# Performance work log

Measured on AMD Instinct MI355X. Metric: run time of the kernel, lower is better.

Reference implementation:

```python
import jax, jax.numpy as jnp
import numpy as np

B, N, F = 8, 2048, 64
H, LAT = 256, 64
K1, K2 = N // 2, N // 4  # DiffPool keeps nodes//2 per stage


def _adj_mm(A, x):
    # A: [N,M] (shared) or [B,N,M] (per-sample); x: [B,M,F]
    if A.ndim == 2:
        return jnp.einsum('nm,bmf->bnf', A, x)
    return jnp.einsum('bnm,bmf->bnf', A, x)


def _gcn(x, A, W, b, act=None):
    # spektral GCNConv: act(A @ (X W) + b)
    h = _adj_mm(A, x @ W) + b
    return act(h) if act is not None else h


def _diffpool(x, A, K_emb, K_pool):
    # spektral DiffPool (linear embedding activation, softmax selection)
    z = _adj_mm(A, x @ K_emb)                               # [B,N,C]
    s = jax.nn.softmax(_adj_mm(A, x @ K_pool), axis=-1)     # [B,N,K]
    x_pool = jnp.einsum('bnk,bnc->bkc', s, z)               # S^T Z
    AS = _adj_mm(A, s)                                       # [B,N,K]
    A_pool = jnp.einsum('bnk,bnl->bkl', s, AS)              # S^T A S
    return x_pool, A_pool, s


def setup_inputs() -> dict:
    key = jax.random.key(0)
    ks = jax.random.split(key, 24)

    def glorot(k, shape):
        return (jax.random.normal(k, shape) * jnp.sqrt(2.0 / (shape[0] + shape[1]))).astype(jnp.float32)

    # symmetric sparse-ish adjacency with self loops, GCN-normalized (keeps activations stable)
    mask = (jax.random.uniform(ks[0], (N, N)) < 0.01).astype(jnp.float32)
    A = jnp.minimum(jnp.maximum(mask, mask.T) + jnp.eye(N, dtype=jnp.float32), 1.0)
    dinv = 1.0 / jnp.sqrt(jnp.sum(A, axis=-1))
    adj = A * dinv[:, None] * dinv[None, :]

    return {
        'x': jax.random.normal(ks[1], (B, N, F), dtype=jnp.float32),
        'eps': jax.random.normal(ks[2], (B, K2, LAT), dtype=jnp.float32),
        'adj': adj,
        'We1': glorot(ks[3], (F, H)), 'be1': jnp.zeros((H,), jnp.float32),
        'Kemb1': glorot(ks[4], (H, H)), 'Kpool1': glorot(ks[5], (H, K1)),
        'We2': glorot(ks[6], (H, H)), 'be2': jnp.zeros((H,), jnp.float32),
        'Kemb2': glorot(ks[7], (H, H)), 'Kpool2': glorot(ks[8], (H, K2)),
        'We3': glorot(ks[9], (H, 2 * LAT)), 'be3': jnp.zeros((2 * LAT,), jnp.float32),
        'Wd0': glorot(ks[10], (LAT, H)), 'bd0': jnp.zeros((H,), jnp.float32),
        'Wd1': glorot(ks[11], (H, H)), 'bd1': jnp.zeros((H,), jnp.float32),
        'Wd2': glorot(ks[12], (H, H)), 'bd2': jnp.zeros((H,), jnp.float32),
        'Wdf': glorot(ks[13], (H, F)), 'bdf': jnp.zeros((F,), jnp.float32),
    }


def reference(x, eps, adj, We1, be1, Kemb1, Kpool1, We2, be2, Kemb2, Kpool2,
              We3, be3, Wd0, bd0, Wd1, bd1, Wd2, bd2, Wdf, bdf):
    A0 = adj
    # ---- encode ----
    h = _gcn(x, A0, We1, be1, jax.nn.relu)              # [B,N,H]
    h, A1, s1 = _diffpool(h, A0, Kemb1, Kpool1)          # [B,K1,H], [B,K1,K1], [B,N,K1]
    h = _gcn(h, A1, We2, be2, jax.nn.relu)
    h, A2, s2 = _diffpool(h, A1, Kemb2, Kpool2)          # [B,K2,H]
    h = _gcn(h, A2, We3, be3, None)                      # [B,K2,2*LAT]
    mean, log_var = jnp.split(h, 2, axis=-1)
    z = mean + jnp.exp(0.5 * log_var) * eps              # reparameterize
    # ---- decode ----
    d = _gcn(z, A2, Wd0, bd0, jax.nn.relu)
    d = jnp.einsum('bnk,bkc->bnc', s2, d)                # DiffUnpool: S @ x
    d = _gcn(d, A1, Wd1, bd1, jax.nn.relu)
    d = jnp.einsum('bnk,bkc->bnc', s1, d)
    d = _gcn(d, A0, Wd2, bd2, jax.nn.relu)
    out = _gcn(d, A0, Wdf, bdf, jax.nn.softplus)         # [B,N,F]
    return out, mean, log_var
```

## Files before the change

### kernel.cpp

```cpp
#include <hip/hip_runtime.h>
#include <math.h>

#define BATCH 8
typedef unsigned short US;

typedef __attribute__((ext_vector_type(8))) short short8;
typedef __attribute__((ext_vector_type(4))) float f32x4;

__device__ __forceinline__ US f2b(float f) {
  union { float f; unsigned u; } v; v.f = f;
  unsigned r = v.u + 0x7fffu + ((v.u >> 16) & 1u);
  return (US)(r >> 16);
}
__device__ __forceinline__ float b2f(US h) {
  union { unsigned u; float f; } v; v.u = ((unsigned)h) << 16;
  return v.f;
}

__device__ __forceinline__ void gload16(const US* g, US* l) {
  __builtin_amdgcn_global_load_lds(
      (const __attribute__((address_space(1))) unsigned int*)g,
      (__attribute__((address_space(3))) unsigned int*)l, 16, 0, 0);
}

__device__ __forceinline__ int lidx2(int r, int ko) {
  return r * 64 + ((((ko >> 3) ^ (r & 7)) << 3));
}

template <int TN, int ACT, int OUT, bool HASBIAS>
__global__ __launch_bounds__(256) void mm_k(
    const US* __restrict__ A, const US* __restrict__ B,
    const float* __restrict__ bias, void* __restrict__ Cv, void* __restrict__ Cv2,
    int M, int N, int K, int lda, long long sA, long long sB, long long sC,
    long long sC2, int gx, int gy) {
  constexpr int JF = TN / 32;
  __shared__ US As[128 * 64];
  __shared__ US Bs[TN * 64];

  const int nb = blockIdx.x;
  const int nb2 = (nb & 7) * (gx * gy) + (nb >> 3);
  const int bx = nb2 % gx;
  const int by = (nb2 / gx) % gy;
  const int b = nb2 / (gx * gy);

  A += (long long)b * sA;
  B += (long long)b * sB;
  const int m0 = by * 128, n0 = bx * TN;
  const int t = threadIdx.x, lane = t & 63, w = t >> 6;
  const int wm = (w >> 1) * 64, wn = (w & 1) * (TN / 2);
  const int l15 = lane & 15, lg = lane >> 4;
  const int lrow = lane >> 3;
  const int gcell = (((lane & 7) ^ lrow) << 3);

  f32x4 acc[4][JF];
#pragma unroll
  for (int i = 0; i < 4; ++i)
#pragma unroll
    for (int j = 0; j < JF; ++j) acc[i][j] = (f32x4){0.f, 0.f, 0.f, 0.f};

  for (int k0 = 0; k0 < K; k0 += 64) {
#pragma unroll
    for (int i = 0; i < 4; ++i) {
      const int g = w * 4 + i;
      gload16(A + (long long)(m0 + g * 8 + lrow) * lda + k0 + gcell, &As[g * 512]);
    }
#pragma unroll
    for (int i = 0; i < TN / 32; ++i) {
      const int g = w * (TN / 32) + i;
      gload16(B + (long long)(n0 + g * 8 + lrow) * K + k0 + gcell, &Bs[g * 512]);
    }
    __syncthreads();

#pragma unroll
    for (int kk = 0; kk < 2; ++kk) {
      const int ko = kk * 32 + lg * 8;
      short8 af[4], bf[JF];
#pragma unroll
      for (int i = 0; i < 4; ++i)
        af[i] = *(const short8*)&As[lidx2(wm + i * 16 + l15, ko)];
#pragma unroll
      for (int j = 0; j < JF; ++j)
        bf[j] = *(const short8*)&Bs[lidx2(wn + j * 16 + l15, ko)];
#pragma unroll
      for (int i = 0; i < 4; ++i)
#pragma unroll
        for (int j = 0; j < JF; ++j)
          acc[i][j] = __builtin_amdgcn_mfma_f32_16x16x32_bf16(af[i], bf[j],
                                                              acc[i][j], 0, 0, 0);
    }
    __syncthreads();
  }

  const long long cb = (long long)b * sC;
  const long long cb2 = (long long)b * sC2;
#pragma unroll
  for (int fj = 0; fj < JF; ++fj) {
    const int col = n0 + wn + fj * 16 + l15;
    const float bsv = HASBIAS ? bias[col] : 0.0f;
#pragma unroll
    for (int fi = 0; fi < 4; ++fi) {
      const int row0 = m0 + wm + fi * 16 + lg * 4;
      float v[4];
#pragma unroll
      for (int e = 0; e < 4; ++e) {
        float x = acc[fi][fj][e] + bsv;
        if (ACT == 1) x = fmaxf(x, 0.0f);
        if (ACT == 2) x = (x > 20.0f) ? x : log1pf(expf(x));
        v[e] = x;
      }
      if (OUT == 1 || OUT == 3) {
        ushort4 pk;
        pk.x = f2b(v[0]); pk.y = f2b(v[1]); pk.z = f2b(v[2]); pk.w = f2b(v[3]);
        US* c2 = (OUT == 3) ? (US*)Cv2 : (US*)Cv;
        *(ushort4*)&c2[cb2 + (long long)col * M + row0] = pk;
      }
      if (OUT == 0 || OUT == 3) {
#pragma unroll
        for (int e = 0; e < 4; ++e)
          ((US*)Cv)[cb + (long long)(row0 + e) * N + col] = f2b(v[e]);
      }
      if (OUT == 2) {
#pragma unroll
        for (int e = 0; e < 4; ++e)
          ((float*)Cv)[cb + (long long)(row0 + e) * N + col] = v[e];
      }
    }
  }
}

template <int OUT>
__global__ __launch_bounds__(512, 1) void mm256_k(
    const US* __restrict__ A, const US* __restrict__ B, void* __restrict__ Cv,
    void* __restrict__ Cv2, int M, int N, int K, int lda, long long sA,
    long long sB, long long sC, long long sC2, int gx, int gy) {
  __shared__ US lds[8][8192];

  const int nb = blockIdx.x;
  const int chunk = gx * gy;
  const int nb2 = (nb & 7) * chunk + (nb >> 3);
  const int bx = nb2 % gx;
  const int by = (nb2 / gx) % gy;
  const int b = nb2 / chunk;

  const int m0 = by * 256, n0 = bx * 256;
  const int tid = threadIdx.x;
  const int lane = tid & 63, w = tid >> 6;
  const int wr = w >> 2, wc = w & 3;
  const int l15 = lane & 15, lg = lane >> 4;

  const US* Ab = A + (long long)b * sA + (long long)m0 * lda;
  const US* Bb = B + (long long)b * sB + (long long)n0 * K;
  const int NT = K >> 6;

  auto stageH = [&](int H) {
    const int s = H >> 2, h = H & 3;
    const int ab = h & 1, kk = h >> 1;
    US* reg = &lds[ab * 4 + (s & 1) * 2 + kk][0];
    const US* src = ab ? Bb : Ab;
    const int ld = ab ? K : lda;
#pragma unroll
    for (int i = 0; i < 2; ++i) {
      const int rbase = (w * 2 + i) * 16;
      const int r = rbase + (lane >> 2);
      const int csrc = (lane & 3) ^ ((r >> 1) & 3);
      gload16(src + (long long)r * ld + s * 64 + kk * 32 + csrc * 8,
              reg + rbase * 32);
    }
  };

  f32x4 acc[8][4];
#pragma unroll
  for (int m = 0; m < 8; ++m)
#pragma unroll
    for (int j = 0; j < 4; ++j) acc[m][j] = (f32x4){0.f, 0.f, 0.f, 0.f};
  short8 a4[4], b4[4];

  for (int H = 0; H < 6; ++H) stageH(H);
  asm volatile("s_waitcnt vmcnt(4)" ::: "memory");
  __builtin_amdgcn_s_barrier();

#define PH(kk_, mh_, DOH, HV, VM, tt)                                          \
  {                                                                            \
    const US* Ar = &lds[((tt) & 1) * 2 + (kk_)][0];                            \
    const US* Br = &lds[4 + ((tt) & 1) * 2 + (kk_)][0];                        \
    _Pragma("unroll") for (int i = 0; i < 4; ++i) {                            \
      const int r = wr * 128 + (mh_) * 64 + i * 16 + l15;                      \
      a4[i] = *(const short8*)&Ar[r * 32 + ((lg ^ ((r >> 1) & 3)) << 3)];      \
    }                                                                          \
    if ((mh_) == 0) {                                                          \
      _Pragma("unroll") for (int j = 0; j < 4; ++j) {                          \
        const int rr = wc * 64 + j * 16 + l15;                                 \
        b4[j] = *(const short8*)&Br[rr * 32 + ((lg ^ ((rr >> 1) & 3)) << 3)];  \
      }                                                                        \
    }                                                                          \
    if (DOH) stageH(HV);                                                       \
    if ((VM) == 1) asm volatile("s_waitcnt vmcnt(4)" ::: "memory");            \
    if ((VM) == 2) asm volatile("s_waitcnt vmcnt(0)" ::: "memory");            \
    __builtin_amdgcn_s_barrier();                                              \
    __builtin_amdgcn_s_setprio(1);                                             \
    _Pragma("unroll") for (int i = 0; i < 4; ++i)                              \
      _Pragma("unroll") for (int j = 0; j < 4; ++j)                            \
        acc[(mh_) * 4 + i][j] = __builtin_amdgcn_mfma_f32_16x16x32_bf16(       \
            a4[i], b4[j], acc[(mh_) * 4 + i][j], 0, 0, 0);                     \
    __builtin_amdgcn_s_setprio(0);                                             \
    __builtin_amdgcn_s_barrier();                                              \
  }

  int t2 = 0;
  for (; t2 < NT - 2; ++t2) {
    PH(0, 0, true, 4 * t2 + 6, 0, t2)
    PH(0, 1, true, 4 * t2 + 7, 0, t2)
    PH(1, 0, true, 4 * t2 + 8, 0, t2)
    PH(1, 1, true, 4 * t2 + 9, 1, t2)
  }
  PH(0, 0, true, 4 * (NT - 2) + 6, 0, NT - 2)
  PH(0, 1, true, 4 * (NT - 2) + 7, 0, NT - 2)
  PH(1, 0, false, 0, 0, NT - 2)
  PH(1, 1, false, 0, 2, NT - 2)
  PH(0, 0, false, 0, 0, NT - 1)
  PH(0, 1, false, 0, 0, NT - 1)
  PH(1, 0, false, 0, 0, NT - 1)
  PH(1, 1, false, 0, 0, NT - 1)
#undef PH

  const long long cb = (long long)b * sC;
  const long long cb2 = (long long)b * sC2;
#pragma unroll
  for (int j = 0; j < 4; ++j) {
    const int col = n0 + wc * 64 + j * 16 + l15;
#pragma unroll
    for (int m = 0; m < 8; ++m) {
      const int row0 = m0 + wr * 128 + m * 16 + lg * 4;
      if (OUT == 1 || OUT == 3) {
        ushort4 pk;
        pk.x = f2b(acc[m][j][0]); pk.y = f2b(acc[m][j][1]);
        pk.z = f2b(acc[m][j][2]); pk.w = f2b(acc[m][j][3]);
        US* c2 = (OUT == 3) ? (US*)Cv2 : (US*)Cv;
        *(ushort4*)&c2[cb2 + (long long)col * M + row0] = pk;
      }
      if (OUT == 0 || OUT == 3) {
#pragma unroll
        for (int e = 0; e < 4; ++e)
          ((US*)Cv)[cb + (long long)(row0 + e) * N + col] = f2b(acc[m][j][e]);
      }
    }
  }
}

template <int ACT, int OUT, bool HASBIAS>
__global__ __launch_bounds__(256) void mm64_k(
    const US* __restrict__ A, const US* __restrict__ B,
    const float* __restrict__ bias, void* __restrict__ Cv,
    int M, int N, int K, int lda, long long sA, long long sB, long long sC,
    int gx, int gy) {
  __shared__ US As[4][4096];
  __shared__ US Bs[4][4096];

  const int nb = blockIdx.x;
  const int chunk = gx * gy;
  const int nb2 = (nb & 7) * chunk + (nb >> 3);
  const int bx = nb2 % gx;
  const int by = (nb2 / gx) % gy;
  const int b = nb2 / chunk;

  const int m0 = by * 64, n0 = bx * 64;
  const int tid = threadIdx.x;
  const int lane = tid & 63, w = tid >> 6;
  const int wr = w >> 1, wc = w & 1;
  const int l15 = lane & 15, lg = lane >> 4;
  const int lrow = lane >> 3;
  const int gcell = (((lane & 7) ^ lrow) << 3);

  const US* Ag = A + (long long)b * sA + (long long)m0 * lda;
  const US* Bg = B + (long long)b * sB + (long long)n0 * K;
  const int NT = K >> 6;

  auto stage = [&](int tt) {
    US* Ad = &As[tt & 3][0];
    US* Bd = &Bs[tt & 3][0];
    const int k0 = tt * 64;
#pragma unroll
    for (int i = 0; i < 2; ++i) {
      const int g = w * 2 + i;
      const int r = g * 8 + lrow;
      gload16(Ag + (long long)r * lda + k0 + gcell, Ad + g * 512);
      gload16(Bg + (long long)r * K + k0 + gcell, Bd + g * 512);
    }
  };

  f32x4 acc[2][2];
#pragma unroll
  for (int i = 0; i < 2; ++i)
#pragma unroll
    for (int j = 0; j < 2; ++j) acc[i][j] = (f32x4){0.f, 0.f, 0.f, 0.f};

  for (int i = 0; i < 3 && i < NT; ++i) stage(i);

  for (int t = 0; t < NT; ++t) {
    if (t + 3 < NT) stage(t + 3);
    const int rem = NT - 1 - t;
    if (rem >= 3) asm volatile("s_waitcnt vmcnt(12)" ::: "memory");
    else if (rem == 2) asm volatile("s_waitcnt vmcnt(8)" ::: "memory");
    else if (rem == 1) asm volatile("s_waitcnt vmcnt(4)" ::: "memory");
    else asm volatile("s_waitcnt vmcnt(0)" ::: "memory");
    asm volatile("s_barrier" ::: "memory");
    const US* Ad = &As[t & 3][0];
    const US* Bd = &Bs[t & 3][0];
#pragma unroll
    for (int kk = 0; kk < 2; ++kk) {
      const int ko = kk * 32 + lg * 8;
      short8 af[2], bf[2];
      af[0] = *(const short8*)&Ad[lidx2(wr * 32 + l15, ko)];
      af[1] = *(const short8*)&Ad[lidx2(wr * 32 + 16 + l15, ko)];
      bf[0] = *(const short8*)&Bd[lidx2(wc * 32 + l15, ko)];
      bf[1] = *(const short8*)&Bd[lidx2(wc * 32 + 16 + l15, ko)];
#pragma unroll
      for (int i = 0; i < 2; ++i)
#pragma unroll
        for (int j = 0; j < 2; ++j)
          acc[i][j] = __builtin_amdgcn_mfma_f32_16x16x32_bf16(af[i], bf[j],
                                                              acc[i][j], 0, 0, 0);
    }
    asm volatile("s_barrier" ::: "memory");
  }

  const long long cb = (long long)b * sC;
#pragma unroll
  for (int fj = 0; fj < 2; ++fj) {
    const int col = n0 + wc * 32 + fj * 16 + l15;
    const float bsv = HASBIAS ? bias[col] : 0.0f;
#pragma unroll
    for (int fi = 0; fi < 2; ++fi) {
      const int row0 = m0 + wr * 32 + fi * 16 + lg * 4;
      float v[4];
#pragma unroll
      for (int e = 0; e < 4; ++e) {
        float x = acc[fi][fj][e] + bsv;
        if (ACT == 1) x = fmaxf(x, 0.0f);
        if (ACT == 2) x = (x > 20.0f) ? x : log1pf(expf(x));
        v[e] = x;
      }
      if (OUT == 1) {
        ushort4 pk;
        pk.x = f2b(v[0]); pk.y = f2b(v[1]); pk.z = f2b(v[2]); pk.w = f2b(v[3]);
        *(ushort4*)&((US*)Cv)[cb + (long long)col * M + row0] = pk;
      } else if (OUT == 0) {
#pragma unroll
        for (int e = 0; e < 4; ++e)
          ((US*)Cv)[cb + (long long)(row0 + e) * N + col] = f2b(v[e]);
      } else {
#pragma unroll
        for (int e = 0; e < 4; ++e)
          ((float*)Cv)[cb + (long long)(row0 + e) * N + col] = v[e];
      }
    }
  }
}

__global__ __launch_bounds__(256) void csr_count_k(const float* __restrict__ adj,
                                                   int* __restrict__ rowcnt) {
  const int row = blockIdx.x, t = threadIdx.x;
  const float* p = adj + (long long)row * 2048;
  int c = 0;
  for (int j = t; j < 2048; j += 256) c += (p[j] != 0.0f);
  __shared__ int red[256];
  red[t] = c;
  __syncthreads();
  for (int s = 128; s; s >>= 1) {
    if (t < s) red[t] += red[t + s];
    __syncthreads();
  }
  if (t == 0) rowcnt[row] = red[0];
}

__global__ __launch_bounds__(256) void csr_scan_k(const int* __restrict__ rowcnt,
                                                  int* __restrict__ rowptr) {
  __shared__ int red[256];
  const int t = threadIdx.x;
  int base = 0;
  for (int ch = 0; ch < 8; ++ch) {
    const int v = rowcnt[ch * 256 + t];
    red[t] = v;
    __syncthreads();
    for (int s = 1; s < 256; s <<= 1) {
      const int add = (t >= s) ? red[t - s] : 0;
      __syncthreads();
      red[t] += add;
      __syncthreads();
    }
    rowptr[ch * 256 + t] = base + red[t] - v;
    const int tot = red[255];
    __syncthreads();
    base += tot;
  }
  if (t == 0) rowptr[2048] = base;
}

__global__ __launch_bounds__(256) void csr_fill_k(const float* __restrict__ adj,
                                                  const int* __restrict__ rowptr,
                                                  int* __restrict__ colidx,
                                                  float* __restrict__ vals) {
  const int row = blockIdx.x, t = threadIdx.x;
  const float* p = adj + (long long)row * 2048;
  int cnt = 0;
  for (int j = t; j < 2048; j += 256) cnt += (p[j] != 0.0f);
  __shared__ int red[256];
  red[t] = cnt;
  __syncthreads();
  for (int s = 1; s < 256; s <<= 1) {
    const int add = (t >= s) ? red[t - s] : 0;
    __syncthreads();
    red[t] += add;
    __syncthreads();
  }
  int off = rowptr[row] + red[t] - cnt;
  for (int j = t; j < 2048; j += 256) {
    const float a = p[j];
    if (a != 0.0f) {
      colidx[off] = j;
      vals[off] = a;
      ++off;
    }
  }
}

template <int COLS, bool INF32, int ACT, bool OUTF32, bool HASBIAS>
__global__ __launch_bounds__(256) void spmm_k(
    const int* __restrict__ rowptr, const int* __restrict__ colidx,
    const float* __restrict__ vals, const void* __restrict__ Xv,
    const float* __restrict__ bias, void* __restrict__ Yv) {
  constexpr int BP = 256 / COLS;
  constexpr int NP = BATCH / BP;
  const int row = blockIdx.x;
  const int t = threadIdx.x;
  const int c = t & (COLS - 1);
  const int bsub = t / COLS;
  const int e0 = rowptr[row], e1 = rowptr[row + 1];
  float acc[NP];
#pragma unroll
  for (int p = 0; p < NP; ++p) acc[p] = 0.0f;
  for (int e = e0; e < e1; ++e) {
    const int j = colidx[e];
    const float a = vals[e];
#pragma unroll
    for (int p = 0; p < NP; ++p) {
      const int b = p * BP + bsub;
      const long long idx = ((long long)b * 2048 + j) * COLS + c;
      const float xv = INF32 ? ((const float*)Xv)[idx] : b2f(((const US*)Xv)[idx]);
      acc[p] += a * xv;
    }
  }
#pragma unroll
  for (int p = 0; p < NP; ++p) {
    const int b = p * BP + bsub;
    float v = acc[p] + (HASBIAS ? bias[c] : 0.0f);
    if (ACT == 2) v = (v > 20.0f) ? v : log1pf(expf(v));
    const long long idx = ((long long)b * 2048 + row) * COLS + c;
    if (OUTF32) ((float*)Yv)[idx] = v;
    else ((US*)Yv)[idx] = f2b(v);
  }
}

template <int RPT>
__global__ __launch_bounds__(256) void sm_partial_k(
    const US* __restrict__ x, float* __restrict__ pm, float* __restrict__ ps,
    int R, int C, long long sB, int NS) {
  const int b = blockIdx.y, blk = blockIdx.x;
  const int cpr = C >> 3;
  const int t = threadIdx.x;
  const int cslot = t & (cpr - 1);
  const int rsub = t / cpr;
  const int nsub = 256 / cpr;
  const int rowsPerBlock = R / NS;
  const int r0 = blk * rowsPerBlock + rsub * RPT;
  const US* p = x + (long long)b * sB + (long long)r0 * C + cslot * 8;
  union { uint4 v; US s[8]; } buf[RPT];
#pragma unroll
  for (int i = 0; i < RPT; ++i) buf[i].v = *(const uint4*)(p + (long long)i * C);
  float M[8], S[8];
#pragma unroll
  for (int j = 0; j < 8; ++j) M[j] = b2f(buf[0].s[j]);
#pragma unroll
  for (int i = 1; i < RPT; ++i)
#pragma unroll
    for (int j = 0; j < 8; ++j) M[j] = fmaxf(M[j], b2f(buf[i].s[j]));
#pragma unroll
  for (int j = 0; j < 8; ++j) S[j] = 0.f;
#pragma unroll
  for (int i = 0; i < RPT; ++i)
#pragma unroll
    for (int j = 0; j < 8; ++j) S[j] += __expf(b2f(buf[i].s[j]) - M[j]);
  const long long pi = (long long)(b * NS + blk) * nsub + rsub;
  float* pmo = pm + pi * C + cslot * 8;
  float* pso = ps + pi * C + cslot * 8;
  *(float4*)pmo = make_float4(M[0], M[1], M[2], M[3]);
  *(float4*)(pmo + 4) = make_float4(M[4], M[5], M[6], M[7]);
  *(float4*)pso = make_float4(S[0], S[1], S[2], S[3]);
  *(float4*)(pso + 4) = make_float4(S[4], S[5], S[6], S[7]);
}

__global__ __launch_bounds__(256) void sm_combine_k(
    const float* __restrict__ pm, const float* __restrict__ ps,
    float* __restrict__ Mf, float* __restrict__ Sinv, int C, int NP) {
  const int b = blockIdx.x, t = threadIdx.x;
  const int cpr = C >> 3;
  if (t >= cpr) return;
  const int c = t * 8;
  const float* pmB = pm + (long long)b * NP * C + c;
  const float* psB = ps + (long long)b * NP * C + c;
  float M[8], S[8];
#pragma unroll
  for (int j = 0; j < 8; ++j) { M[j] = pmB[j]; S[j] = psB[j]; }
  for (int e = 1; e < NP; ++e) {
    const float* pme = pmB + (long long)e * C;
    const float* pse = psB + (long long)e * C;
#pragma unroll
    for (int j = 0; j < 8; ++j) {
      const float m2 = pme[j], s2 = pse[j];
      const float nm = fmaxf(M[j], m2);
      S[j] = S[j] * __expf(M[j] - nm) + s2 * __expf(m2 - nm);
      M[j] = nm;
    }
  }
#pragma unroll
  for (int j = 0; j < 8; ++j) {
    Mf[(long long)b * C + c + j] = M[j];
    Sinv[(long long)b * C + c + j] = 1.0f / S[j];
  }
}

template <int RPT>
__global__ __launch_bounds__(256) void sm_norm_k(
    US* __restrict__ x, const float* __restrict__ Mf,
    const float* __restrict__ Sinv, int R, int C, long long sB, int NS) {
  const int b = blockIdx.y, blk = blockIdx.x;
  const int cpr = C >> 3;
  const int t = threadIdx.x;
  const int cslot = t & (cpr - 1);
  const int rsub = t / cpr;
  const int rowsPerBlock = R / NS;
  const int r0 = blk * rowsPerBlock + rsub * RPT;
  US* p = x + (long long)b * sB + (long long)r0 * C + cslot * 8;
  float M[8], Si[8];
#pragma unroll
  for (int j = 0; j < 8; ++j) {
    M[j] = Mf[(long long)b * C + cslot * 8 + j];
    Si[j] = Sinv[(long long)b * C + cslot * 8 + j];
  }
#pragma unroll
  for (int i = 0; i < RPT; ++i) {
    union { uint4 v; US s[8]; } buf;
    buf.v = *(const uint4*)(p + (long long)i * C);
#pragma unroll
    for (int j = 0; j < 8; ++j)
      buf.s[j] = f2b(__expf(b2f(buf.s[j]) - M[j]) * Si[j]);
    *(uint4*)(p + (long long)i * C) = buf.v;
  }
}

struct WT { const float* src; US* dst; int R, C, tileOff; };
struct WTab { WT e[11]; };

__global__ __launch_bounds__(256) void wtrans_k(WTab tab) {
  __shared__ US L[64][65];
  const int tile = blockIdx.x;
  int i = 0;
#pragma unroll
  for (int j = 1; j < 11; ++j)
    if (tab.e[j].tileOff <= tile) i = j;
  const WT w = tab.e[i];
  const int lt = tile - w.tileOff;
  const int tc = w.C / 64;
  const int r0 = (lt / tc) * 64, c0 = (lt % tc) * 64;
  const int t = threadIdx.x;
  const int lr = t >> 4, lc = (t & 15) * 4;
#pragma unroll
  for (int k = 0; k < 4; ++k) {
    const int rr = r0 + lr + 16 * k;
    const float4 v = *(const float4*)&w.src[(long long)rr * w.C + c0 + lc];
    L[lr + 16 * k][lc + 0] = f2b(v.x);
    L[lr + 16 * k][lc + 1] = f2b(v.y);
    L[lr + 16 * k][lc + 2] = f2b(v.z);
    L[lr + 16 * k][lc + 3] = f2b(v.w);
  }
  __syncthreads();
#pragma unroll
  for (int k = 0; k < 4; ++k) {
    ushort4 o;
    o.x = L[lc + 0][lr + 16 * k];
    o.y = L[lc + 1][lr + 16 * k];
    o.z = L[lc + 2][lr + 16 * k];
    o.w = L[lc + 3][lr + 16 * k];
    *(ushort4*)&w.dst[(long long)(c0 + lr + 16 * k) * w.R + r0 + lc] = o;
  }
}

__global__ __launch_bounds__(256) void f2b_k(const float* __restrict__ s,
                                             US* __restrict__ d, int n4) {
  const int i = blockIdx.x * 256 + threadIdx.x;
  if (i < n4) {
    const float4 v = ((const float4*)s)[i];
    ushort4 o;
    o.x = f2b(v.x); o.y = f2b(v.y); o.z = f2b(v.z); o.w = f2b(v.w);
    ((ushort4*)d)[i] = o;
  }
}

__global__ __launch_bounds__(256) void reparam_k(
    const float* __restrict__ h3, const float* __restrict__ eps,
    float* __restrict__ om, float* __restrict__ olv, US* __restrict__ z,
    int total) {
  const int i = blockIdx.x * 256 + threadIdx.x;
  if (i >= total) return;
  const int j = i & 63;
  const long long r = i >> 6;
  const float m = h3[r * 128 + j];
  const float lv = h3[r * 128 + 64 + j];
  om[i] = m;
  olv[i] = lv;
  z[i] = f2b(m + expf(0.5f * lv) * eps[i]);
}

static void mm(hipStream_t st, const US* A, const US* B, const float* bias,
               void* C, void* C2, int M, int N, int K, int lda, long long sA,
               long long sB, long long sC, long long sC2, int act, int outm,
               int tn) {
  const int gx = N / tn, gy = M / 128;
  dim3 g(gx * gy * BATCH), blk(256);
#define L(TN, ACT, OUT, HB) \
  mm_k<TN, ACT, OUT, HB><<<g, blk, 0, st>>>(A, B, bias, C, C2, M, N, K, lda, sA, sB, sC, sC2, gx, gy)
  if (tn == 64) {
    if (outm == 0) L(64, 0, 0, false);
    else if (outm == 1) L(64, 0, 1, false);
    else L(64, 2, 2, true);
  } else {
    if (outm == 0) {
      if (act == 1) L(128, 1, 0, true);
      else L(128, 0, 0, false);
    } else if (outm == 1) {
      if (act == 1) L(128, 1, 1, true);
      else L(128, 0, 1, false);
    } else if (outm == 2) L(128, 0, 2, true);
    else L(128, 0, 3, false);
  }
#undef L
}

static void mm256(hipStream_t st, const US* A, const US* B, void* C, void* C2,
                  int M, int N, int K, int lda, long long sA, long long sB,
                  long long sC, long long sC2, int outm) {
  const int gx = N / 256, gy = M / 256;
  dim3 g(gx * gy * BATCH), blk(512);
  if (outm == 0)
    mm256_k<0><<<g, blk, 0, st>>>(A, B, C, C2, M, N, K, lda, sA, sB, sC, sC2, gx, gy);
  else if (outm == 1)
    mm256_k<1><<<g, blk, 0, st>>>(A, B, C, C2, M, N, K, lda, sA, sB, sC, sC2, gx, gy);
  else
    mm256_k<3><<<g, blk, 0, st>>>(A, B, C, C2, M, N, K, lda, sA, sB, sC, sC2, gx, gy);
}

static void mm64(hipStream_t st, const US* A, const US* B, const float* bias,
                 void* C, int M, int N, int K, int lda, long long sA,
                 long long sB, long long sC, int act, int outm) {
  const int gx = N / 64, gy = M / 64;
  dim3 g(gx * gy * BATCH), blk(256);
  if (outm == 0)
    mm64_k<0, 0, false><<<g, blk, 0, st>>>(A, B, nullptr, C, M, N, K, lda, sA, sB, sC, gx, gy);
  else if (outm == 1)
    mm64_k<0, 1, false><<<g, blk, 0, st>>>(A, B, nullptr, C, M, N, K, lda, sA, sB, sC, gx, gy);
  else
    mm64_k<2, 2, true><<<g, blk, 0, st>>>(A, B, bias, C, M, N, K, lda, sA, sB, sC, gx, gy);
}

extern "C" void kernel_launch(void* const* d_in, const int* in_sizes, int n_in,
                              void* d_out, int out_size, void* d_ws, size_t ws_size,
                              hipStream_t stream) {
  const float* x      = (const float*)d_in[0];
  const float* eps    = (const float*)d_in[1];
  const float* adj    = (const float*)d_in[2];
  const float* We1    = (const float*)d_in[3];
  const float* be1    = (const float*)d_in[4];
  const float* Kemb1  = (const float*)d_in[5];
  const float* Kpool1 = (const float*)d_in[6];
  const float* We2    = (const float*)d_in[7];
  const float* be2    = (const float*)d_in[8];
  const float* Kemb2  = (const float*)d_in[9];
  const float* Kpool2 = (const float*)d_in[10];
  const float* We3    = (const float*)d_in[11];
  const float* be3    = (const float*)d_in[12];
  const float* Wd0    = (const float*)d_in[13];
  const float* bd0    = (const float*)d_in[14];
  const float* Wd1    = (const float*)d_in[15];
  const float* bd1    = (const float*)d_in[16];
  const float* Wd2    = (const float*)d_in[17];
  const float* bd2    = (const float*)d_in[18];
  const float* Wdf    = (const float*)d_in[19];
  const float* bdf    = (const float*)d_in[20];
  (void)in_sizes; (void)n_in; (void)ws_size; (void)out_size;

  float* out = (float*)d_out;
  float* out_mean = out + (long long)8 * 2048 * 64;
  float* out_lv = out_mean + (long long)8 * 512 * 64;

  char* base = (char*)d_ws;
  size_t off = 0;
  auto alloc = [&](size_t bytes) {
    char* p = base + off;
    off += (bytes + 255) & ~(size_t)255;
    return p;
  };
  US* adjb = (US*)alloc(2048LL * 2048 * 2);
  US* Y0   = (US*)alloc(8LL * 2048 * 64 * 2);
  US* h1b  = (US*)alloc(8LL * 2048 * 256 * 2);
  US* g1   = (US*)alloc(8LL * 2048 * 256 * 2);
  US* R1   = (US*)alloc(8LL * 2304 * 2048 * 2);
  US* AS1  = (US*)alloc(8LL * 2048 * 1024 * 2);
  US* P1o  = (US*)alloc(8LL * 1024 * 1280 * 2);
  US* t1T  = (US*)alloc(8LL * 256 * 1024 * 2);
  US* h2T  = (US*)alloc(8LL * 256 * 1024 * 2);
  US* g2   = (US*)alloc(8LL * 1024 * 256 * 2);
  US* R2   = (US*)alloc(8LL * 1280 * 1024 * 2);
  US* AS2  = (US*)alloc(8LL * 1024 * 512 * 2);
  US* P2o  = (US*)alloc(8LL * 512 * 768 * 2);
  US* t2T  = (US*)alloc(8LL * 128 * 512 * 2);
  float* h3f = (float*)alloc(8LL * 512 * 128 * 4);
  US* zlb  = (US*)alloc(8LL * 512 * 64 * 2);
  US* t3T  = (US*)alloc(8LL * 256 * 512 * 2);
  US* d0   = (US*)alloc(8LL * 512 * 256 * 2);
  US* t4T  = (US*)alloc(8LL * 256 * 512 * 2);
  US* d2   = (US*)alloc(8LL * 1024 * 256 * 2);
  US* t5T  = (US*)alloc(8LL * 256 * 1024 * 2);
  US* d4   = (US*)alloc(8LL * 2048 * 256 * 2);
  US* t6   = (US*)alloc(8LL * 2048 * 64 * 2);
  float* pm   = (float*)alloc(8LL * 128 * 2048 * 4);
  float* ps   = (float*)alloc(8LL * 128 * 2048 * 4);
  float* Mf   = (float*)alloc(8LL * 2048 * 4);
  float* Sinv = (float*)alloc(8LL * 2048 * 4);
  int* rowcnt = (int*)alloc(2048 * 4);
  int* rowptr = (int*)alloc(2049 * 4);
  int* colidx = (int*)alloc(2048LL * 256 * 4);
  float* vals = (float*)alloc(2048LL * 256 * 4);
  US* We1T  = (US*)alloc(256 * 64 * 2);
  US* KpKe1 = (US*)alloc(1280 * 256 * 2);
  US* We2T  = (US*)alloc(256 * 256 * 2);
  US* KpKe2 = (US*)alloc(768 * 256 * 2);
  US* We3T  = (US*)alloc(128 * 256 * 2);
  US* Wd0T  = (US*)alloc(256 * 64 * 2);
  US* Wd1T  = (US*)alloc(256 * 256 * 2);
  US* Wd2T  = (US*)alloc(256 * 256 * 2);
  US* WdfT  = (US*)alloc(64 * 256 * 2);

  f2b_k<<<dim3(2048 * 2048 / 4 / 256), dim3(256), 0, stream>>>(adj, adjb, 2048 * 2048 / 4);
  {
    WTab tab;
    int toff = 0, i = 0;
    auto add = [&](const float* s, US* d, int R, int C) {
      tab.e[i++] = WT{s, d, R, C, toff};
      toff += (R / 64) * (C / 64);
    };
    add(We1, We1T, 64, 256);
    add(Kpool1, KpKe1, 256, 1024);
    add(Kemb1, KpKe1 + 1024 * 256, 256, 256);
    add(We2, We2T, 256, 256);
    add(Kpool2, KpKe2, 256, 512);
    add(Kemb2, KpKe2 + 512 * 256, 256, 256);
    add(We3, We3T, 256, 128);
    add(Wd0, Wd0T, 64, 256);
    add(Wd1, Wd1T, 256, 256);
    add(Wd2, Wd2T, 256, 256);
    add(Wdf, WdfT, 256, 64);
    wtrans_k<<<dim3(toff), dim3(256), 0, stream>>>(tab);
  }
  csr_count_k<<<dim3(2048), dim3(256), 0, stream>>>(adj, rowcnt);
  csr_scan_k<<<dim3(1), dim3(256), 0, stream>>>(rowcnt, rowptr);
  csr_fill_k<<<dim3(2048), dim3(256), 0, stream>>>(adj, rowptr, colidx, vals);

  const long long SR1 = 2304LL * 2048, SR2 = 1280LL * 1024;
  US* s1T  = R1;
  US* B1   = R1 + 1024 * 2048;
  US* AS1T = R1 + 1280 * 2048;
  US* s2T  = R2;
  US* B2   = R2 + 512 * 1024;
  US* AS2T = R2 + 768 * 1024;
  US* A1c  = P1o + 256;
  US* A2c  = P2o + 256;

  spmm_k<64, true, 0, false, false><<<dim3(2048), dim3(256), 0, stream>>>(
      rowptr, colidx, vals, x, nullptr, Y0);
  mm(stream, Y0, We1T, be1, h1b, nullptr, 2048, 256, 64, 64, 2048LL * 64, 0,
     2048LL * 256, 0, 1, 0, 128);
  spmm_k<256, false, 0, false, false><<<dim3(2048), dim3(256), 0, stream>>>(
      rowptr, colidx, vals, h1b, nullptr, g1);
  mm256(stream, g1, KpKe1, R1, nullptr, 2048, 1280, 256, 256, 2048LL * 256, 0,
        SR1, SR1, 1);
  sm_partial_k<8><<<dim3(128, 8), dim3(256), 0, stream>>>(s1T, pm, ps, 1024, 2048, SR1, 128);
  sm_combine_k<<<dim3(8), dim3(256), 0, stream>>>(pm, ps, Mf, Sinv, 2048, 128);
  sm_norm_k<8><<<dim3(128, 8), dim3(256), 0, stream>>>(s1T, Mf, Sinv, 1024, 2048, SR1, 128);
  mm256(stream, adjb, s1T, AS1, AS1T, 2048, 1024, 2048, 2048, 0, SR1,
        2048LL * 1024, SR1, 3);
  mm256(stream, s1T, B1, P1o, nullptr, 1024, 1280, 2048, 2048, SR1, SR1,
        1024LL * 1280, 0, 0);
  mm(stream, P1o, We2T, nullptr, t1T, nullptr, 1024, 256, 256, 1280, 1024LL * 1280,
     0, 0, 256LL * 1024, 0, 1, 128);
  mm(stream, A1c, t1T, be2, h2T, nullptr, 1024, 256, 1024, 1280, 1024LL * 1280,
     256LL * 1024, 0, 256LL * 1024, 1, 1, 128);
  mm(stream, A1c, h2T, nullptr, g2, nullptr, 1024, 256, 1024, 1280, 1024LL * 1280,
     256LL * 1024, 1024LL * 256, 0, 0, 0, 128);
  mm(stream, g2, KpKe2, nullptr, R2, nullptr, 1024, 768, 256, 256, 1024LL * 256,
     0, 0, SR2, 0, 1, 128);
  sm_partial_k<4><<<dim3(64, 8), dim3(256), 0, stream>>>(s2T, pm, ps, 512, 1024, SR2, 64);
  sm_combine_k<<<dim3(8), dim3(256), 0, stream>>>(pm, ps, Mf, Sinv, 1024, 128);
  sm_norm_k<4><<<dim3(64, 8), dim3(256), 0, stream>>>(s2T, Mf, Sinv, 512, 1024, SR2, 64);
  mm(stream, A1c, s2T, nullptr, AS2, AS2T, 1024, 512, 1024, 1280, 1024LL * 1280,
     SR2, 1024LL * 512, SR2, 0, 3, 128);
  mm(stream, s2T, B2, nullptr, P2o, nullptr, 512, 768, 1024, 1024, SR2, SR2,
     512LL * 768, 0, 0, 0, 128);
  mm(stream, P2o, We3T, nullptr, t2T, nullptr, 512, 128, 256, 768, 512LL * 768,
     0, 0, 128LL * 512, 0, 1, 128);
  mm(stream, A2c, t2T, be3, h3f, nullptr, 512, 128, 512, 768, 512LL * 768,
     128LL * 512, 512LL * 128, 0, 0, 2, 128);
  reparam_k<<<dim3(8 * 512 * 64 / 256), dim3(256), 0, stream>>>(h3f, eps, out_mean,
                                                                out_lv, zlb, 8 * 512 * 64);

  mm(stream, zlb, Wd0T, nullptr, t3T, nullptr, 512, 256, 64, 64, 512LL * 64, 0, 0,
     256LL * 512, 0, 1, 128);
  mm(stream, A2c, t3T, bd0, d0, nullptr, 512, 256, 512, 768, 512LL * 768,
     256LL * 512, 512LL * 256, 0, 1, 0, 128);
  mm(stream, d0, Wd1T, nullptr, t4T, nullptr, 512, 256, 256, 256, 512LL * 256, 0,
     0, 256LL * 512, 0, 1, 128);
  mm(stream, AS2, t4T, bd1, d2, nullptr, 1024, 256, 512, 512, 1024LL * 512,
     256LL * 512, 1024LL * 256, 0, 1, 0, 128);
  mm(stream, d2, Wd2T, nullptr, t5T, nullptr, 1024, 256, 256, 256, 1024LL * 256, 0,
     0, 256LL * 1024, 0, 1, 128);
  mm(stream, AS1, t5T, bd2, d4, nullptr, 2048, 256, 1024, 1024, 2048LL * 1024,
     256LL * 1024, 2048LL * 256, 0, 1, 0, 128);
  mm64(stream, d4, WdfT, nullptr, t6, 2048, 64, 256, 256, 2048LL * 256, 0,
       2048LL * 64, 0, 0);
  spmm_k<64, false, 2, true, true><<<dim3(2048), dim3(256), 0, stream>>>(
      rowptr, colidx, vals, t6, bdf, out);
}
```

Measured before the change: 702.4 us.

## Replace dense A·S GEMM with CSR SpMM and row-wise softmax on untransposed scores

The first DiffPool's assignment matrix product A·S was computed as a dense 2048x2048 bf16 GEMM. It is now computed with a CSR sparse-matrix kernel that exploits the roughly 1% density of the adjacency, which also removes the adjacency-to-bf16 conversion. The score GEMM now writes row-major output, and a per-row block softmax replaces the three-kernel partial, combine and normalize softmax. Explicit transpose kernels then rebuild the transposed layouts that later GEMMs expect, and some scratch buffers are aliased into the new region. This trades a large dense GEMM for irregular gathers plus two extra transpose passes over the data.

```diff
diff --git a/kernel.cpp b/kernel.cpp
--- a/kernel.cpp
+++ b/kernel.cpp
@@ -461,6 +461,72 @@
   }
 }
 
+__global__ __launch_bounds__(256) void spmm1024_k(
+    const int* __restrict__ rowptr, const int* __restrict__ colidx,
+    const float* __restrict__ vals, const US* __restrict__ X, int ldx,
+    long long sX, US* __restrict__ Y) {
+  const int bid = blockIdx.x;
+  const int b = bid & 7;
+  const int row = bid >> 3;
+  const int t = threadIdx.x;
+  const int c0 = t * 4;
+  const US* Xb = X + (long long)b * sX;
+  const int e0 = rowptr[row], e1 = rowptr[row + 1];
+  float acc[4] = {0.f, 0.f, 0.f, 0.f};
+  for (int e = e0; e < e1; ++e) {
+    const int j = colidx[e];
+    const float a = vals[e];
+    const ushort4 xv = *(const ushort4*)&Xb[(long long)j * ldx + c0];
+    acc[0] += a * b2f(xv.x);
+    acc[1] += a * b2f(xv.y);
+    acc[2] += a * b2f(xv.z);
+    acc[3] += a * b2f(xv.w);
+  }
+  ushort4 o;
+  o.x = f2b(acc[0]); o.y = f2b(acc[1]); o.z = f2b(acc[2]); o.w = f2b(acc[3]);
+  *(ushort4*)&Y[((long long)b * 2048 + row) * 1024 + c0] = o;
+}
+
+__global__ __launch_bounds__(256) void rowsm_k(US* __restrict__ x, int ldx,
+                                               long long sB) {
+  __shared__ float red[256];
+  const int bid = blockIdx.x;
+  const int b = bid & 7;
+  const int row = bid >> 3;
+  const int t = threadIdx.x;
+  US* p = x + (long long)b * sB + (long long)row * ldx + t * 4;
+  union { ushort4 v; US s[4]; } buf;
+  buf.v = *(const ushort4*)p;
+  float v[4];
+#pragma unroll
+  for (int i = 0; i < 4; ++i) v[i] = b2f(buf.s[i]);
+  float mx = fmaxf(fmaxf(v[0], v[1]), fmaxf(v[2], v[3]));
+  red[t] = mx;
+  __syncthreads();
+  for (int s = 128; s; s >>= 1) {
+    if (t < s) red[t] = fmaxf(red[t], red[t + s]);
+    __syncthreads();
+  }
+  mx = red[0];
+  __syncthreads();
+  float sum = 0.f;
+#pragma unroll
+  for (int i = 0; i < 4; ++i) {
+    v[i] = __expf(v[i] - mx);
+    sum += v[i];
+  }
+  red[t] = sum;
+  __syncthreads();
+  for (int s = 128; s; s >>= 1) {
+    if (t < s) red[t] += red[t + s];
+    __syncthreads();
+  }
+  const float inv = 1.0f / red[0];
+#pragma unroll
+  for (int i = 0; i < 4; ++i) buf.s[i] = f2b(v[i] * inv);
+  *(ushort4*)p = buf.v;
+}
+
 template <int RPT>
 __global__ __launch_bounds__(256) void sm_partial_k(
     const US* __restrict__ x, float* __restrict__ pm, float* __restrict__ ps,
@@ -558,6 +624,37 @@
   }
 }
 
+__global__ __launch_bounds__(256) void transb_k(const US* __restrict__ src,
+                                                US* __restrict__ dst, int R,
+                                                int C, long long sIn,
+                                                long long sOut) {
+  __shared__ US L[64][65];
+  const int b = blockIdx.z;
+  const int r0 = blockIdx.y * 64, c0 = blockIdx.x * 64;
+  const int t = threadIdx.x;
+  const int lr = t >> 4, lc = (t & 15) * 4;
+  const US* s = src + (long long)b * sIn;
+#pragma unroll
+  for (int i = 0; i < 4; ++i) {
+    const int rr = r0 + lr + 16 * i;
+    const ushort4 v = *(const ushort4*)&s[(long long)rr * C + c0 + lc];
+    L[lr + 16 * i][lc + 0] = v.x;
+    L[lr + 16 * i][lc + 1] = v.y;
+    L[lr + 16 * i][lc + 2] = v.z;
+    L[lr + 16 * i][lc + 3] = v.w;
+  }
+  __syncthreads();
+#pragma unroll
+  for (int i = 0; i < 4; ++i) {
+    ushort4 o;
+    o.x = L[lc + 0][lr + 16 * i];
+    o.y = L[lc + 1][lr + 16 * i];
+    o.z = L[lc + 2][lr + 16 * i];
+    o.w = L[lc + 3][lr + 16 * i];
+    *(ushort4*)&dst[(long long)b * sOut + (long long)(c0 + lr + 16 * i) * R + r0 + lc] = o;
+  }
+}
+
 struct WT { const float* src; US* dst; int R, C, tileOff; };
 struct WTab { WT e[11]; };
 
@@ -592,17 +689,6 @@
     o.z = L[lc + 2][lr + 16 * k];
     o.w = L[lc + 3][lr + 16 * k];
     *(ushort4*)&w.dst[(long long)(c0 + lr + 16 * k) * w.R + r0 + lc] = o;
-  }
-}
-
-__global__ __launch_bounds__(256) void f2b_k(const float* __restrict__ s,
-                                             US* __restrict__ d, int n4) {
-  const int i = blockIdx.x * 256 + threadIdx.x;
-  if (i < n4) {
-    const float4 v = ((const float4*)s)[i];
-    ushort4 o;
-    o.x = f2b(v.x); o.y = f2b(v.y); o.z = f2b(v.z); o.w = f2b(v.w);
-    ((ushort4*)d)[i] = o;
   }
 }
 
@@ -709,10 +795,19 @@
     off += (bytes + 255) & ~(size_t)255;
     return p;
   };
-  US* adjb = (US*)alloc(2048LL * 2048 * 2);
   US* Y0   = (US*)alloc(8LL * 2048 * 64 * 2);
   US* h1b  = (US*)alloc(8LL * 2048 * 256 * 2);
   US* g1   = (US*)alloc(8LL * 2048 * 256 * 2);
+  US* R1n  = (US*)alloc(8LL * 2048 * 1280 * 2);
+  float* pm = (float*)R1n;
+  float* ps = pm + 8LL * 128 * 2048;
+  US* d4    = (US*)(ps + 8LL * 128 * 2048);
+  US* t5T   = d4 + 8LL * 2048 * 256;
+  US* d2    = t5T + 8LL * 256 * 1024;
+  US* t3T   = d2 + 8LL * 1024 * 256;
+  US* t4T   = t3T + 8LL * 256 * 512;
+  US* d0    = t4T + 8LL * 256 * 512;
+  US* t6    = d0 + 8LL * 512 * 256;
   US* R1   = (US*)alloc(8LL * 2304 * 2048 * 2);
   US* AS1  = (US*)alloc(8LL * 2048 * 1024 * 2);
   US* P1o  = (US*)alloc(8LL * 1024 * 1280 * 2);
@@ -725,15 +820,6 @@
   US* t2T  = (US*)alloc(8LL * 128 * 512 * 2);
   float* h3f = (float*)alloc(8LL * 512 * 128 * 4);
   US* zlb  = (US*)alloc(8LL * 512 * 64 * 2);
-  US* t3T  = (US*)alloc(8LL * 256 * 512 * 2);
-  US* d0   = (US*)alloc(8LL * 512 * 256 * 2);
-  US* t4T  = (US*)alloc(8LL * 256 * 512 * 2);
-  US* d2   = (US*)alloc(8LL * 1024 * 256 * 2);
-  US* t5T  = (US*)alloc(8LL * 256 * 1024 * 2);
-  US* d4   = (US*)alloc(8LL * 2048 * 256 * 2);
-  US* t6   = (US*)alloc(8LL * 2048 * 64 * 2);
-  float* pm   = (float*)alloc(8LL * 128 * 2048 * 4);
-  float* ps   = (float*)alloc(8LL * 128 * 2048 * 4);
   float* Mf   = (float*)alloc(8LL * 2048 * 4);
   float* Sinv = (float*)alloc(8LL * 2048 * 4);
   int* rowcnt = (int*)alloc(2048 * 4);
@@ -750,7 +836,6 @@
   US* Wd2T  = (US*)alloc(256 * 256 * 2);
   US* WdfT  = (US*)alloc(64 * 256 * 2);
 
-  f2b_k<<<dim3(2048 * 2048 / 4 / 256), dim3(256), 0, stream>>>(adj, adjb, 2048 * 2048 / 4);
   {
     WTab tab;
     int toff = 0, i = 0;
@@ -776,6 +861,7 @@
   csr_fill_k<<<dim3(2048), dim3(256), 0, stream>>>(adj, rowptr, colidx, vals);
 
   const long long SR1 = 2304LL * 2048, SR2 = 1280LL * 1024;
+  const long long SR1n = 2048LL * 1280;
   US* s1T  = R1;
   US* B1   = R1 + 1024 * 2048;
   US* AS1T = R1 + 1280 * 2048;
@@ -791,13 +877,15 @@
      2048LL * 256, 0, 1, 0, 128);
   spmm_k<256, false, 0, false, false><<<dim3(2048), dim3(256), 0, stream>>>(
       rowptr, colidx, vals, h1b, nullptr, g1);
-  mm256(stream, g1, KpKe1, R1, nullptr, 2048, 1280, 256, 256, 2048LL * 256, 0,
-        SR1, SR1, 1);
-  sm_partial_k<8><<<dim3(128, 8), dim3(256), 0, stream>>>(s1T, pm, ps, 1024, 2048, SR1, 128);
-  sm_combine_k<<<dim3(8), dim3(256), 0, stream>>>(pm, ps, Mf, Sinv, 2048, 128);
-  sm_norm_k<8><<<dim3(128, 8), dim3(256), 0, stream>>>(s1T, Mf, Sinv, 1024, 2048, SR1, 128);
-  mm256(stream, adjb, s1T, AS1, AS1T, 2048, 1024, 2048, 2048, 0, SR1,
-        2048LL * 1024, SR1, 3);
+  mm256(stream, g1, KpKe1, R1n, nullptr, 2048, 1280, 256, 256, 2048LL * 256, 0,
+        SR1n, 0, 0);
+  rowsm_k<<<dim3(16384), dim3(256), 0, stream>>>(R1n, 1280, SR1n);
+  transb_k<<<dim3(20, 32, 8), dim3(256), 0, stream>>>(R1n, R1, 2048, 1280,
+                                                      SR1n, SR1);
+  spmm1024_k<<<dim3(16384), dim3(256), 0, stream>>>(rowptr, colidx, vals, R1n,
+                                                    1280, SR1n, AS1);
+  transb_k<<<dim3(16, 32, 8), dim3(256), 0, stream>>>(AS1, AS1T, 2048, 1024,
+                                                      2048LL * 1024, SR1);
   mm256(stream, s1T, B1, P1o, nullptr, 1024, 1280, 2048, 2048, SR1, SR1,
         1024LL * 1280, 0, 0);
   mm(stream, P1o, We2T, nullptr, t1T, nullptr, 1024, 256, 256, 1280, 1024LL * 1280,
```

Result: faster. 663.6 us (-5.5%).
